# Optimization experiments

Measured on AMD Instinct MI355X. Metric: run time of the kernel, lower is better.

## Reference

```python
import jax, jax.numpy as jnp
import numpy as np

NQ = 4  # n_qubits
C64 = jnp.complex64
INV_SQRT2 = np.float32(1.0 / np.sqrt(2.0))
H_GATE = jnp.array([[1.0, 1.0], [1.0, -1.0]], dtype=C64) * INV_SQRT2


def _apply_1q(state, U, q):
    # state: (B, 2,2,2,2) complex; U: (2,2) shared or (B,2,2) per-batch
    s = jnp.moveaxis(state, q + 1, -1)
    if U.ndim == 2:
        s = jnp.einsum('b...i,ji->b...j', s, U)
    else:
        s = jnp.einsum('b...i,bji->b...j', s, U)
    return jnp.moveaxis(s, -1, q + 1)


def _apply_cnot(state, c, t):
    s = jnp.moveaxis(state, (c + 1, t + 1), (-2, -1))
    s = jnp.stack([s[..., 0, :], s[..., 1, ::-1]], axis=-2)  # flip target when control=1
    return jnp.moveaxis(s, (-2, -1), (c + 1, t + 1))


def _ry(theta):
    co = jnp.cos(theta * 0.5).astype(C64)
    si = jnp.sin(theta * 0.5).astype(C64)
    return jnp.stack([jnp.stack([co, -si], -1), jnp.stack([si, co], -1)], -2)


def _rz(theta):
    e = jnp.exp(-0.5j * theta).astype(C64)
    z = jnp.zeros_like(e)
    return jnp.stack([jnp.stack([e, z], -1), jnp.stack([z, jnp.conj(e)], -1)], -2)


def _rx(theta):
    co = jnp.cos(theta * 0.5).astype(C64)
    si = (-1j * jnp.sin(theta * 0.5)).astype(C64)
    return jnp.stack([jnp.stack([co, si], -1), jnp.stack([si, co], -1)], -2)


def _vqc(y, w):
    # y: (B, NQ) float angles-to-encode; w: (n_qlayers, 3, NQ)
    B = y.shape[0]
    state = jnp.zeros((B, 2 ** NQ), C64).at[:, 0].set(1.0).reshape((B,) + (2,) * NQ)
    ry_ang = jnp.arctan(y)
    rz_ang = jnp.arctan(y * y)
    # encoding: H, RY(arctan y), RZ(arctan y^2) on each wire
    for q in range(NQ):
        state = _apply_1q(state, H_GATE, q)
        state = _apply_1q(state, _ry(ry_ang[:, q]), q)
        state = _apply_1q(state, _rz(rz_ang[:, q]), q)
    # ansatz layers: CNOT ring (n_esteps=1), then RX/RY/RZ with weights
    for l in range(w.shape[0]):
        for q in range(NQ):
            state = _apply_cnot(state, q, (q + 1) % NQ)
        for q in range(NQ):
            state = _apply_1q(state, _rx(w[l, 0, q]), q)
            state = _apply_1q(state, _ry(w[l, 1, q]), q)
            state = _apply_1q(state, _rz(w[l, 2, q]), q)
    probs = state.real ** 2 + state.imag ** 2  # (B,2,2,2,2)
    outs = []
    for q in range(NQ):
        p = jnp.moveaxis(probs, q + 1, 1).reshape(B, 2, -1).sum(-1)
        outs.append(p[:, 0] - p[:, 1])  # <Z_q>
    return jnp.stack(outs, -1).astype(y.dtype)


def _qlstm(x, W_in, b_in, W_out, b_out, w_f, w_i, w_u, w_o):
    B = x.shape[0]
    Hdim = W_out.shape[1]
    h0 = jnp.zeros((B, Hdim), x.dtype)
    c0 = jnp.zeros((B, Hdim), x.dtype)

    def step(carry, x_t):
        h, c = carry
        y = jnp.concatenate([h, x_t], axis=1) @ W_in + b_in  # (B, NQ)
        f = jax.nn.sigmoid(_vqc(y, w_f) @ W_out + b_out)
        i = jax.nn.sigmoid(_vqc(y, w_i) @ W_out + b_out)
        g = jnp.tanh(_vqc(y, w_u) @ W_out + b_out)
        o = jax.nn.sigmoid(_vqc(y, w_o) @ W_out + b_out)
        c = f * c + i * g
        h = o * jnp.tanh(c)
        return (h, c), h

    (hT, cT), outs = jax.lax.scan(step, (h0, c0), jnp.swapaxes(x, 0, 1))
    return jnp.swapaxes(outs, 0, 1), hT, cT


def setup_inputs() -> dict:
    key = jax.random.key(0)
    ks = jax.random.split(key, 9)
    B, S, D, Hdim = 512, 256, 64, 128
    x = jax.random.normal(ks[0], (B, S, D), jnp.float32)
    W_in = jax.random.normal(ks[1], (Hdim + D, NQ), jnp.float32) * 0.1
    b_in = jax.random.normal(ks[2], (NQ,), jnp.float32) * 0.1
    W_out = jax.random.normal(ks[3], (NQ, Hdim), jnp.float32) * 0.1
    b_out = jax.random.normal(ks[4], (Hdim,), jnp.float32) * 0.1
    two_pi = np.float32(2.0 * np.pi)
    w_f = jax.random.uniform(ks[5], (1, 3, NQ), jnp.float32, 0.0, two_pi)
    w_i = jax.random.uniform(ks[6], (1, 3, NQ), jnp.float32, 0.0, two_pi)
    w_u = jax.random.uniform(ks[7], (1, 3, NQ), jnp.float32, 0.0, two_pi)
    w_o = jax.random.uniform(ks[8], (1, 3, NQ), jnp.float32, 0.0, two_pi)
    return {'x': x, 'W_in': W_in, 'b_in': b_in, 'W_out': W_out, 'b_out': b_out,
            'w_f': w_f, 'w_i': w_i, 'w_u': w_u, 'w_o': w_o}


def reference(x, W_in, b_in, W_out, b_out, w_f, w_i, w_u, w_o):
    return _qlstm(x, W_in, b_in, W_out, b_out, w_f, w_i, w_u, w_o)
```

## Files before the change

kernel.cpp:

```cpp
#include <hip/hip_runtime.h>
#include <math.h>

#define B_TOT 512
#define S_LEN 256
#define D_IN  64
#define HDIM  128

typedef float v2f __attribute__((ext_vector_type(2)));

__device__ __forceinline__ float rcp_f(float x) { return __builtin_amdgcn_rcpf(x); }
__device__ __forceinline__ float rsq_f(float x) { return __builtin_amdgcn_rsqf(x); }

__device__ __forceinline__ v2f fma2(v2f a, v2f b, v2f c) { return __builtin_elementwise_fma(a, b, c); }
__device__ __forceinline__ v2f splat2(float s) { v2f r = {s, s}; return r; }

__device__ __forceinline__ v2f sig2(v2f s) {
    v2f e = { __expf(-s.x), __expf(-s.y) };
    v2f ONE = {1.f, 1.f};
    v2f d = e + ONE;
    v2f r = { rcp_f(d.x), rcp_f(d.y) };
    return r;
}
__device__ __forceinline__ v2f tanh2(v2f s) {
    v2f t = s + s;
    v2f e = { __expf(t.x), __expf(t.y) };
    v2f ONE = {1.f, 1.f};
    v2f d = e + ONE;
    v2f r = { rcp_f(d.x), rcp_f(d.y) };
    v2f NTWO = {-2.f, -2.f};
    return fma2(r, NTWO, ONE);
}

template<int CTRL>
__device__ __forceinline__ float dpp_add(float v) {
    int t = __builtin_amdgcn_update_dpp(0, __float_as_int(v), CTRL, 0xF, 0xF, true);
    return v + __int_as_float(t);
}

__device__ __forceinline__ float gsum32(float v) {
    v = dpp_add<0xB1>(v);
    v = dpp_add<0x4E>(v);
    v = dpp_add<0x141>(v);
    v = dpp_add<0x140>(v);
    int s = __builtin_amdgcn_ds_swizzle(__float_as_int(v), 0x401F);
    return v + __int_as_float(s);
}

__global__ void __launch_bounds__(64, 1) qlstm_kernel(
    const float* __restrict__ x,
    const float* __restrict__ Win,
    const float* __restrict__ bin,
    const float* __restrict__ Wout,
    const float* __restrict__ bout,
    const float* __restrict__ wf,
    const float* __restrict__ wi,
    const float* __restrict__ wu,
    const float* __restrict__ wo,
    float* __restrict__ out)
{
    const int l  = threadIdx.x;
    const int j  = l & 31;
    const int bb = l >> 5;
    const int b  = blockIdx.x * 2 + bb;

    const float4* W4 = reinterpret_cast<const float4*>(Win);
    v2f whA[4], whB[4];
#pragma unroll
    for (int k = 0; k < 4; ++k) {
        float4 r = W4[j + 32 * k];
        whA[k].x = r.x; whA[k].y = r.y;
        whB[k].x = r.z; whB[k].y = r.w;
    }
    float4 rx0 = W4[128 + 2 * j];
    float4 rx1 = W4[128 + 2 * j + 1];
    v2f wxA0 = {rx0.x, rx0.y}, wxB0 = {rx0.z, rx0.w};
    v2f wxA1 = {rx1.x, rx1.y}, wxB1 = {rx1.z, rx1.w};
    const float4 bn4 = *reinterpret_cast<const float4*>(bin);
    const v2f bnA = {bn4.x * 0.03125f, bn4.y * 0.03125f};
    const v2f bnB = {bn4.z * 0.03125f, bn4.w * 0.03125f};

    v2f WoA[4], WoB[4];
#pragma unroll
    for (int q = 0; q < 4; ++q) {
        WoA[q].x = Wout[q * HDIM + j];      WoA[q].y = Wout[q * HDIM + j + 32];
        WoB[q].x = Wout[q * HDIM + j + 64]; WoB[q].y = Wout[q * HDIM + j + 96];
    }
    v2f boA = {bout[j],      bout[j + 32]};
    v2f boB = {bout[j + 64], bout[j + 96]};

    v2f UX[4][2], UY[4][2], UZ[4][2];
    {
        const float* wg[4] = {wf, wi, wu, wo};
#pragma unroll
        for (int g = 0; g < 4; ++g) {
#pragma unroll
            for (int p = 0; p < 2; ++p) {
#pragma unroll
                for (int e = 0; e < 2; ++e) {
                    int q = 2 * p + e;
                    float a  = wg[g][q];
                    float be = wg[g][4 + q];
                    float sa = sinf(a),  ca = cosf(a);
                    float sb = sinf(be), cb = cosf(be);
                    UX[g][p][e] = -sb;
                    UY[g][p][e] = cb * sa;
                    UZ[g][p][e] = cb * ca;
                }
            }
        }
    }

    v2f hA = {0.f, 0.f}, hB = {0.f, 0.f};
    v2f cA = {0.f, 0.f}, cB = {0.f, 0.f};

    const float* xb = x + (size_t)b * (S_LEN * D_IN) + 2 * j;
    float* ob = out + (size_t)b * (S_LEN * HDIM) + j;

    const v2f ONE = {1.f, 1.f};

    auto step = [&](v2f xf, int t) {
        v2f pa01 = fma2(splat2(xf.x), wxA0, bnA);
        v2f pa23 = fma2(splat2(xf.x), wxB0, bnB);
        pa01 = fma2(splat2(xf.y), wxA1, pa01);
        pa23 = fma2(splat2(xf.y), wxB1, pa23);
        v2f pb01 = splat2(hA.x) * whA[0];
        v2f pb23 = splat2(hA.x) * whB[0];
        pb01 = fma2(splat2(hA.y), whA[1], pb01);
        pb23 = fma2(splat2(hA.y), whB[1], pb23);
        v2f pc01 = splat2(hB.x) * whA[2];
        v2f pc23 = splat2(hB.x) * whB[2];
        pc01 = fma2(splat2(hB.y), whA[3], pc01);
        pc23 = fma2(splat2(hB.y), whB[3], pc23);
        v2f p01 = (pa01 + pb01) + pc01;
        v2f p23 = (pa23 + pb23) + pc23;

        float y0 = gsum32(p01.x);
        float y1 = gsum32(p01.y);
        float y2 = gsum32(p23.x);
        float y3 = gsum32(p23.y);

        v2f yA = {y0, y1}, yB = {y2, y3};
        v2f qA = yA * yA,  qB = yB * yB;
        v2f aA = fma2(yA, yA, ONE), aB = fma2(yB, yB, ONE);
        v2f bA = fma2(qA, qA, ONE), bB = fma2(qB, qB, ONE);
        v2f r1A = { rsq_f(aA.x), rsq_f(aA.y) };
        v2f r1B = { rsq_f(aB.x), rsq_f(aB.y) };
        v2f r2A = { rsq_f(bA.x), rsq_f(bA.y) };
        v2f r2B = { rsq_f(bB.x), rsq_f(bB.y) };
        v2f nxA = r1A * r2A, nxB = r1B * r2B;
        v2f nyA = qA * nxA,  nyB = qB * nxB;
        v2f nzA = -(yA * r1A), nzB = -(yB * r1B);
        float nx0 = nxA.x, nx1 = nxA.y, nx2 = nxB.x, nx3 = nxB.y;
        float ny0 = nyA.x, ny1 = nyA.y, ny2 = nyB.x, ny3 = nyB.y;
        float nz0 = nzA.x, nz1 = nzA.y, nz2 = nzB.x, nz3 = nzB.y;

        float nz01 = nz0 * nz1;
        float nz23 = nz2 * nz3;
        v2f TXa, TXb, TYa, TYb, TZa, TZb;
        TXa.x = nx0 * nx1;  TXa.y = nx1 * nx2;
        TXb.x = nx2 * nx3;  TXb.y = TXa.x * nx3;
        TZa.x = nz1 * nz23; TZa.y = nz01;
        TZb.x = nz01 * nz2; TZb.y = nz01 * nz23;
        TYa.x = (nx0 * ny1) * nz23;  TYa.y = (nz0 * ny1) * nx2;
        TYb.x = (nz01 * ny2) * nx3;  TYb.y = -(ny0 * ny1) * (nz2 * ny3);

        v2f preA[4], preB[4];
#pragma unroll
        for (int g = 0; g < 4; ++g) {
            v2f za = fma2(UX[g][0], TXa, fma2(UY[g][0], TYa, UZ[g][0] * TZa));
            v2f zb = fma2(UX[g][1], TXb, fma2(UY[g][1], TYb, UZ[g][1] * TZb));
            v2f sA = fma2(splat2(za.x), WoA[0], boA);
            sA = fma2(splat2(za.y), WoA[1], sA);
            sA = fma2(splat2(zb.x), WoA[2], sA);
            sA = fma2(splat2(zb.y), WoA[3], sA);
            v2f sB = fma2(splat2(za.x), WoB[0], boB);
            sB = fma2(splat2(za.y), WoB[1], sB);
            sB = fma2(splat2(zb.x), WoB[2], sB);
            sB = fma2(splat2(zb.y), WoB[3], sB);
            preA[g] = sA; preB[g] = sB;
        }

        v2f fA = sig2(preA[0]),  fB = sig2(preB[0]);
        v2f iA = sig2(preA[1]),  iB = sig2(preB[1]);
        v2f gA = tanh2(preA[2]), gB = tanh2(preB[2]);
        v2f oA = sig2(preA[3]),  oB = sig2(preB[3]);
        cA = fma2(fA, cA, iA * gA);
        cB = fma2(fB, cB, iB * gB);
        hA = oA * tanh2(cA);
        hB = oB * tanh2(cB);

        float* op = ob + (size_t)t * HDIM;
        op[0]  = hA.x;
        op[32] = hA.y;
        op[64] = hB.x;
        op[96] = hB.y;
    };

    v2f xc0 = *reinterpret_cast<const v2f*>(xb + (size_t)0 * D_IN);
    v2f xc1 = *reinterpret_cast<const v2f*>(xb + (size_t)1 * D_IN);
    v2f xn0 = *reinterpret_cast<const v2f*>(xb + (size_t)2 * D_IN);
    v2f xn1 = *reinterpret_cast<const v2f*>(xb + (size_t)3 * D_IN);

    for (int grp = 0; grp < S_LEN / 2; ++grp) {
        step(xc0, 2 * grp);
        step(xc1, 2 * grp + 1);
        xc0 = xn0; xc1 = xn1;
        int t0 = 2 * grp + 4; if (t0 > S_LEN - 1) t0 = S_LEN - 1;
        int t1 = 2 * grp + 5; if (t1 > S_LEN - 1) t1 = S_LEN - 1;
        xn0 = *reinterpret_cast<const v2f*>(xb + (size_t)t0 * D_IN);
        xn1 = *reinterpret_cast<const v2f*>(xb + (size_t)t1 * D_IN);
    }

    float* hT = out + (size_t)B_TOT * S_LEN * HDIM;
    float* cT = hT + (size_t)B_TOT * HDIM;
    float* hp = hT + (size_t)b * HDIM + j;
    float* cp = cT + (size_t)b * HDIM + j;
    hp[0]  = hA.x; hp[32] = hA.y; hp[64] = hB.x; hp[96] = hB.y;
    cp[0]  = cA.x; cp[32] = cA.y; cp[64] = cB.x; cp[96] = cB.y;
}

extern "C" void kernel_launch(void* const* d_in, const int* in_sizes, int n_in,
                              void* d_out, int out_size, void* d_ws, size_t ws_size,
                              hipStream_t stream) {
    qlstm_kernel<<<dim3(B_TOT / 2), dim3(64), 0, stream>>>(
        (const float*)d_in[0],
        (const float*)d_in[1],
        (const float*)d_in[2],
        (const float*)d_in[3],
        (const float*)d_in[4],
        (const float*)d_in[5],
        (const float*)d_in[6],
        (const float*)d_in[7],
        (const float*)d_in[8],
        (float*)d_out);
}
```

Before: 249.0 us.

## Precompute input projection in separate kernel and give each batch a full wave

Adds a separate kernel that computes the x-dependent part of the input projection for all timesteps ahead of time and stores it in workspace. The recurrent kernel then only does the h-dependent dot product per step. The recurrent kernel now uses one 64-lane wave per batch element instead of two batches per wave, which doubles the grid and halves per-lane work. In exchange, each step's reduction gains a 64-wide bpermute stage, there is an extra launch, and the workspace array must be written and read back.

```diff
diff --git a/kernel.cpp b/kernel.cpp
--- a/kernel.cpp
+++ b/kernel.cpp
@@ -37,15 +37,51 @@
     return v + __int_as_float(t);
 }
 
-__device__ __forceinline__ float gsum32(float v) {
+__device__ __forceinline__ float allsum64(float v, int idx32) {
     v = dpp_add<0xB1>(v);
     v = dpp_add<0x4E>(v);
     v = dpp_add<0x141>(v);
     v = dpp_add<0x140>(v);
     int s = __builtin_amdgcn_ds_swizzle(__float_as_int(v), 0x401F);
-    return v + __int_as_float(s);
-}
-
+    v += __int_as_float(s);
+    int t = __builtin_amdgcn_ds_bpermute(idx32, __float_as_int(v));
+    v += __int_as_float(t);
+    return v;
+}
+
+__global__ void __launch_bounds__(64, 1) xproj_kernel(
+    const float* __restrict__ x,
+    const float* __restrict__ Win,
+    const float* __restrict__ bin,
+    float4* __restrict__ yx)
+{
+    const int l  = threadIdx.x;
+    const int b  = blockIdx.x >> 4;
+    const int t0 = (blockIdx.x & 15) << 4;
+    const int idx32 = (l ^ 32) << 2;
+
+    const float4 wx = reinterpret_cast<const float4*>(Win)[128 + l];
+    const v2f wxa = {wx.x, wx.y}, wxb = {wx.z, wx.w};
+    const float4 bn = *reinterpret_cast<const float4*>(bin);
+
+    const float* xp = x + ((size_t)b * S_LEN + t0) * D_IN + l;
+    float4* yp = yx + (size_t)b * S_LEN + t0;
+
+#pragma unroll 4
+    for (int tt = 0; tt < 16; ++tt) {
+        float xv = xp[(size_t)tt * D_IN];
+        v2f p01 = splat2(xv) * wxa;
+        v2f p23 = splat2(xv) * wxb;
+        float y0 = allsum64(p01.x, idx32);
+        float y1 = allsum64(p01.y, idx32);
+        float y2 = allsum64(p23.x, idx32);
+        float y3 = allsum64(p23.y, idx32);
+        if (l == 0)
+            yp[tt] = make_float4(y0 + bn.x, y1 + bn.y, y2 + bn.z, y3 + bn.w);
+    }
+}
+
+template<bool PRE>
 __global__ void __launch_bounds__(64, 1) qlstm_kernel(
     const float* __restrict__ x,
     const float* __restrict__ Win,
@@ -56,37 +92,35 @@
     const float* __restrict__ wi,
     const float* __restrict__ wu,
     const float* __restrict__ wo,
-    float* __restrict__ out)
+    float* __restrict__ out,
+    const float4* __restrict__ yx)
 {
-    const int l  = threadIdx.x;
-    const int j  = l & 31;
-    const int bb = l >> 5;
-    const int b  = blockIdx.x * 2 + bb;
+    const int l = threadIdx.x;
+    const int b = blockIdx.x;
+    const int idx32 = (l ^ 32) << 2;
 
     const float4* W4 = reinterpret_cast<const float4*>(Win);
-    v2f whA[4], whB[4];
-#pragma unroll
-    for (int k = 0; k < 4; ++k) {
-        float4 r = W4[j + 32 * k];
-        whA[k].x = r.x; whA[k].y = r.y;
-        whB[k].x = r.z; whB[k].y = r.w;
-    }
-    float4 rx0 = W4[128 + 2 * j];
-    float4 rx1 = W4[128 + 2 * j + 1];
-    v2f wxA0 = {rx0.x, rx0.y}, wxB0 = {rx0.z, rx0.w};
-    v2f wxA1 = {rx1.x, rx1.y}, wxB1 = {rx1.z, rx1.w};
-    const float4 bn4 = *reinterpret_cast<const float4*>(bin);
-    const v2f bnA = {bn4.x * 0.03125f, bn4.y * 0.03125f};
-    const v2f bnB = {bn4.z * 0.03125f, bn4.w * 0.03125f};
-
-    v2f WoA[4], WoB[4];
+    const float4 r0 = W4[2 * l];
+    const float4 r1 = W4[2 * l + 1];
+    const v2f wh0a = {r0.x, r0.y}, wh0b = {r0.z, r0.w};
+    const v2f wh1a = {r1.x, r1.y}, wh1b = {r1.z, r1.w};
+
+    v2f wxa = {0.f, 0.f}, wxb = {0.f, 0.f}, bna = {0.f, 0.f}, bnb = {0.f, 0.f};
+    if (!PRE) {
+        const float4 rx = W4[128 + l];
+        wxa.x = rx.x; wxa.y = rx.y; wxb.x = rx.z; wxb.y = rx.w;
+        const float4 bn = *reinterpret_cast<const float4*>(bin);
+        bna.x = bn.x * 0.015625f; bna.y = bn.y * 0.015625f;
+        bnb.x = bn.z * 0.015625f; bnb.y = bn.w * 0.015625f;
+    }
+
+    v2f Wo[4];
 #pragma unroll
     for (int q = 0; q < 4; ++q) {
-        WoA[q].x = Wout[q * HDIM + j];      WoA[q].y = Wout[q * HDIM + j + 32];
-        WoB[q].x = Wout[q * HDIM + j + 64]; WoB[q].y = Wout[q * HDIM + j + 96];
-    }
-    v2f boA = {bout[j],      bout[j + 32]};
-    v2f boB = {bout[j + 64], bout[j + 96]};
+        Wo[q].x = Wout[q * HDIM + 2 * l];
+        Wo[q].y = Wout[q * HDIM + 2 * l + 1];
+    }
+    const v2f bo = {bout[2 * l], bout[2 * l + 1]};
 
     v2f UX[4][2], UY[4][2], UZ[4][2];
     {
@@ -110,36 +144,47 @@
         }
     }
 
-    v2f hA = {0.f, 0.f}, hB = {0.f, 0.f};
-    v2f cA = {0.f, 0.f}, cB = {0.f, 0.f};
-
-    const float* xb = x + (size_t)b * (S_LEN * D_IN) + 2 * j;
-    float* ob = out + (size_t)b * (S_LEN * HDIM) + j;
-
+    v2f h = {0.f, 0.f}, c = {0.f, 0.f};
     const v2f ONE = {1.f, 1.f};
 
-    auto step = [&](v2f xf, int t) {
-        v2f pa01 = fma2(splat2(xf.x), wxA0, bnA);
-        v2f pa23 = fma2(splat2(xf.x), wxB0, bnB);
-        pa01 = fma2(splat2(xf.y), wxA1, pa01);
-        pa23 = fma2(splat2(xf.y), wxB1, pa23);
-        v2f pb01 = splat2(hA.x) * whA[0];
-        v2f pb23 = splat2(hA.x) * whB[0];
-        pb01 = fma2(splat2(hA.y), whA[1], pb01);
-        pb23 = fma2(splat2(hA.y), whB[1], pb23);
-        v2f pc01 = splat2(hB.x) * whA[2];
-        v2f pc23 = splat2(hB.x) * whB[2];
-        pc01 = fma2(splat2(hB.y), whA[3], pc01);
-        pc23 = fma2(splat2(hB.y), whB[3], pc23);
-        v2f p01 = (pa01 + pb01) + pc01;
-        v2f p23 = (pa23 + pb23) + pc23;
-
-        float y0 = gsum32(p01.x);
-        float y1 = gsum32(p01.y);
-        float y2 = gsum32(p23.x);
-        float y3 = gsum32(p23.y);
+    float* ob = out + (size_t)b * (S_LEN * HDIM) + 2 * l;
+
+    const float4* yxp = PRE ? (yx + (size_t)b * S_LEN) : nullptr;
+    const float*  xb  = PRE ? nullptr : (x + (size_t)b * (S_LEN * D_IN) + l);
+    float4 ya, yb;
+    float  xa, xv_b;
+    if (PRE) { ya = yxp[0]; yb = yxp[1]; }
+    else     { xa = xb[0];  xv_b = xb[D_IN]; }
+
+    for (int t = 0; t < S_LEN; ++t) {
+        v2f p01, p23;
+        float4 ycur;
+        if (PRE) {
+            ycur = ya; ya = yb;
+            int tn = t + 2; if (tn > S_LEN - 1) tn = S_LEN - 1;
+            yb = yxp[tn];
+            p01 = fma2(splat2(h.y), wh1a, splat2(h.x) * wh0a);
+            p23 = fma2(splat2(h.y), wh1b, splat2(h.x) * wh0b);
+        } else {
+            float xv = xa; xa = xv_b;
+            int tn = t + 2; if (tn > S_LEN - 1) tn = S_LEN - 1;
+            xv_b = xb[(size_t)tn * D_IN];
+            p01 = fma2(splat2(h.y), wh1a, fma2(splat2(h.x), wh0a, fma2(splat2(xv), wxa, bna)));
+            p23 = fma2(splat2(h.y), wh1b, fma2(splat2(h.x), wh0b, fma2(splat2(xv), wxb, bnb)));
+        }
+
+        float y0 = allsum64(p01.x, idx32);
+        float y1 = allsum64(p01.y, idx32);
+        float y2 = allsum64(p23.x, idx32);
+        float y3 = allsum64(p23.y, idx32);
 
         v2f yA = {y0, y1}, yB = {y2, y3};
+        if (PRE) {
+            v2f xc0 = {ycur.x, ycur.y}, xc1 = {ycur.z, ycur.w};
+            yA = yA + xc0;
+            yB = yB + xc1;
+        }
+
         v2f qA = yA * yA,  qB = yB * yB;
         v2f aA = fma2(yA, yA, ONE), aB = fma2(yB, yB, ONE);
         v2f bA = fma2(qA, qA, ONE), bB = fma2(qB, qB, ONE);
@@ -164,73 +209,54 @@
         TYa.x = (nx0 * ny1) * nz23;  TYa.y = (nz0 * ny1) * nx2;
         TYb.x = (nz01 * ny2) * nx3;  TYb.y = -(ny0 * ny1) * (nz2 * ny3);
 
-        v2f preA[4], preB[4];
+        v2f pre[4];
 #pragma unroll
         for (int g = 0; g < 4; ++g) {
             v2f za = fma2(UX[g][0], TXa, fma2(UY[g][0], TYa, UZ[g][0] * TZa));
             v2f zb = fma2(UX[g][1], TXb, fma2(UY[g][1], TYb, UZ[g][1] * TZb));
-            v2f sA = fma2(splat2(za.x), WoA[0], boA);
-            sA = fma2(splat2(za.y), WoA[1], sA);
-            sA = fma2(splat2(zb.x), WoA[2], sA);
-            sA = fma2(splat2(zb.y), WoA[3], sA);
-            v2f sB = fma2(splat2(za.x), WoB[0], boB);
-            sB = fma2(splat2(za.y), WoB[1], sB);
-            sB = fma2(splat2(zb.x), WoB[2], sB);
-            sB = fma2(splat2(zb.y), WoB[3], sB);
-            preA[g] = sA; preB[g] = sB;
-        }
-
-        v2f fA = sig2(preA[0]),  fB = sig2(preB[0]);
-        v2f iA = sig2(preA[1]),  iB = sig2(preB[1]);
-        v2f gA = tanh2(preA[2]), gB = tanh2(preB[2]);
-        v2f oA = sig2(preA[3]),  oB = sig2(preB[3]);
-        cA = fma2(fA, cA, iA * gA);
-        cB = fma2(fB, cB, iB * gB);
-        hA = oA * tanh2(cA);
-        hB = oB * tanh2(cB);
-
-        float* op = ob + (size_t)t * HDIM;
-        op[0]  = hA.x;
-        op[32] = hA.y;
-        op[64] = hB.x;
-        op[96] = hB.y;
-    };
-
-    v2f xc0 = *reinterpret_cast<const v2f*>(xb + (size_t)0 * D_IN);
-    v2f xc1 = *reinterpret_cast<const v2f*>(xb + (size_t)1 * D_IN);
-    v2f xn0 = *reinterpret_cast<const v2f*>(xb + (size_t)2 * D_IN);
-    v2f xn1 = *reinterpret_cast<const v2f*>(xb + (size_t)3 * D_IN);
-
-    for (int grp = 0; grp < S_LEN / 2; ++grp) {
-        step(xc0, 2 * grp);
-        step(xc1, 2 * grp + 1);
-        xc0 = xn0; xc1 = xn1;
-        int t0 = 2 * grp + 4; if (t0 > S_LEN - 1) t0 = S_LEN - 1;
-        int t1 = 2 * grp + 5; if (t1 > S_LEN - 1) t1 = S_LEN - 1;
-        xn0 = *reinterpret_cast<const v2f*>(xb + (size_t)t0 * D_IN);
-        xn1 = *reinterpret_cast<const v2f*>(xb + (size_t)t1 * D_IN);
+            v2f s = fma2(splat2(za.x), Wo[0], bo);
+            s = fma2(splat2(za.y), Wo[1], s);
+            s = fma2(splat2(zb.x), Wo[2], s);
+            s = fma2(splat2(zb.y), Wo[3], s);
+            pre[g] = s;
+        }
+
+        v2f fg = sig2(pre[0]);
+        v2f ig = sig2(pre[1]);
+        v2f gg = tanh2(pre[2]);
+        v2f og = sig2(pre[3]);
+        c = fma2(fg, c, ig * gg);
+        h = og * tanh2(c);
+
+        *reinterpret_cast<v2f*>(ob + (size_t)t * HDIM) = h;
     }
 
     float* hT = out + (size_t)B_TOT * S_LEN * HDIM;
     float* cT = hT + (size_t)B_TOT * HDIM;
-    float* hp = hT + (size_t)b * HDIM + j;
-    float* cp = cT + (size_t)b * HDIM + j;
-    hp[0]  = hA.x; hp[32] = hA.y; hp[64] = hB.x; hp[96] = hB.y;
-    cp[0]  = cA.x; cp[32] = cA.y; cp[64] = cB.x; cp[96] = cB.y;
+    *reinterpret_cast<v2f*>(hT + (size_t)b * HDIM + 2 * l) = h;
+    *reinterpret_cast<v2f*>(cT + (size_t)b * HDIM + 2 * l) = c;
 }
 
 extern "C" void kernel_launch(void* const* d_in, const int* in_sizes, int n_in,
                               void* d_out, int out_size, void* d_ws, size_t ws_size,
                               hipStream_t stream) {
-    qlstm_kernel<<<dim3(B_TOT / 2), dim3(64), 0, stream>>>(
-        (const float*)d_in[0],
-        (const float*)d_in[1],
-        (const float*)d_in[2],
-        (const float*)d_in[3],
-        (const float*)d_in[4],
-        (const float*)d_in[5],
-        (const float*)d_in[6],
-        (const float*)d_in[7],
-        (const float*)d_in[8],
-        (float*)d_out);
-}
+    const size_t yx_bytes = (size_t)B_TOT * S_LEN * 4 * sizeof(float);
+    if (d_ws != nullptr && ws_size >= yx_bytes) {
+        float4* yx = (float4*)d_ws;
+        xproj_kernel<<<dim3(B_TOT * 16), dim3(64), 0, stream>>>(
+            (const float*)d_in[0], (const float*)d_in[1], (const float*)d_in[2], yx);
+        qlstm_kernel<true><<<dim3(B_TOT), dim3(64), 0, stream>>>(
+            (const float*)d_in[0], (const float*)d_in[1], (const float*)d_in[2],
+            (const float*)d_in[3], (const float*)d_in[4],
+            (const float*)d_in[5], (const float*)d_in[6],
+            (const float*)d_in[7], (const float*)d_in[8],
+            (float*)d_out, yx);
+    } else {
+        qlstm_kernel<false><<<dim3(B_TOT), dim3(64), 0, stream>>>(
+            (const float*)d_in[0], (const float*)d_in[1], (const float*)d_in[2],
+            (const float*)d_in[3], (const float*)d_in[4],
+            (const float*)d_in[5], (const float*)d_in[6],
+            (const float*)d_in[7], (const float*)d_in[8],
+            (float*)d_out, nullptr);
+    }
+}
```

New measurement: 239.6 us. 3.8% less time.
